# Performance work log

Measured on AMD Instinct MI355X. Metric: run time of the kernel, lower is better.

Reference implementation:

```python
import jax, jax.numpy as jnp
import numpy as np

N = 50000   # nodes per graph
E = 800000  # edges per graph (even, message() splits in half)
F = 100     # node/edge feature dim (init_count_size / init_emb_size)
D = 64      # hidden_dim3 = rule_graph_dim
W_SCALE = 0.05


def _mlp(x, w1, b1, w2, b2):
    return jax.nn.relu(x @ w1 + b1) @ w2 + b2


def _triple_conv(x, src, dst, ea, lw, lb, l2w, l2b, nn_fn):
    # PyG flow source_to_target: x_j = x[edge_index[0]], x_i = x[edge_index[1]]
    h = ea.shape[0] // 2
    x_j = x[src]
    x_i = x[dst]
    m1 = jax.nn.relu(jnp.concatenate([x_i[:h], ea[:h], x_j[:h]], 1) @ lw + lb)
    m2 = jax.nn.relu(jnp.concatenate([x_j[h:], ea[h:], x_i[h:]], 1) @ l2w + l2b)
    msgs = jnp.concatenate([m1, m2], 0)
    agg = jax.ops.segment_sum(msgs, dst, num_segments=x.shape[0])
    # eps = 0.0 buffer -> out = agg + (1+eps)*x = agg + x
    return nn_fn(agg + x)


def setup_inputs() -> dict:
    key = jax.random.key(0)
    ks = jax.random.split(key, 32)
    inp = {
        'features_1': jax.random.normal(ks[0], (N, F), jnp.float32),
        'edge_index_1': jax.random.randint(ks[1], (2, E), 0, N, jnp.int64 if jax.config.jax_enable_x64 else jnp.int32).astype(jnp.int32),
        'edge_attr_1': jax.random.normal(ks[2], (E, F), jnp.float32),
        'features_2': jax.random.normal(ks[3], (N, F), jnp.float32),
        'edge_index_2': jax.random.randint(ks[4], (2, E), 0, N, jnp.int32),
        'edge_attr_2': jax.random.normal(ks[5], (E, F), jnp.float32),
        'c1_lin_w': jax.random.normal(ks[6], (3 * F, F), jnp.float32) * W_SCALE,
        'c1_lin_b': jax.random.normal(ks[7], (F,), jnp.float32) * W_SCALE,
        'c1_lin2_w': jax.random.normal(ks[8], (3 * F, F), jnp.float32) * W_SCALE,
        'c1_lin2_b': jax.random.normal(ks[9], (F,), jnp.float32) * W_SCALE,
        'mlp1_w1': jax.random.normal(ks[10], (F, F), jnp.float32) * W_SCALE,
        'mlp1_b1': jax.random.normal(ks[11], (F,), jnp.float32) * W_SCALE,
        'mlp1_w2': jax.random.normal(ks[12], (F, F), jnp.float32) * W_SCALE,
        'mlp1_b2': jax.random.normal(ks[13], (F,), jnp.float32) * W_SCALE,
        'c2_lin_w': jax.random.normal(ks[14], (3 * F, F), jnp.float32) * W_SCALE,
        'c2_lin_b': jax.random.normal(ks[15], (F,), jnp.float32) * W_SCALE,
        'c2_lin2_w': jax.random.normal(ks[16], (3 * F, F), jnp.float32) * W_SCALE,
        'c2_lin2_b': jax.random.normal(ks[17], (F,), jnp.float32) * W_SCALE,
        'mlp2_w1': jax.random.normal(ks[18], (F, D), jnp.float32) * W_SCALE,
        'mlp2_b1': jax.random.normal(ks[19], (D,), jnp.float32) * W_SCALE,
        'mlp2_w2': jax.random.normal(ks[20], (D, D), jnp.float32) * W_SCALE,
        'mlp2_b2': jax.random.normal(ks[21], (D,), jnp.float32) * W_SCALE,
    }
    return inp


def reference(features_1, edge_index_1, edge_attr_1,
              features_2, edge_index_2, edge_attr_2,
              c1_lin_w, c1_lin_b, c1_lin2_w, c1_lin2_b,
              mlp1_w1, mlp1_b1, mlp1_w2, mlp1_b2,
              c2_lin_w, c2_lin_b, c2_lin2_w, c2_lin2_b,
              mlp2_w1, mlp2_b1, mlp2_w2, mlp2_b2):

    def conv_pass(x, ei, ea):
        src, dst = ei[0], ei[1]
        x = _triple_conv(x, src, dst, ea, c1_lin_w, c1_lin_b, c1_lin2_w, c1_lin2_b,
                         lambda z: _mlp(z, mlp1_w1, mlp1_b1, mlp1_w2, mlp1_b2))
        x = jax.nn.relu(x)
        x = _triple_conv(x, src, dst, ea, c2_lin_w, c2_lin_b, c2_lin2_w, c2_lin2_b,
                         lambda z: _mlp(z, mlp2_w1, mlp2_b1, mlp2_w2, mlp2_b2))
        return x

    f1 = conv_pass(features_1, edge_index_1, edge_attr_1)  # [N, D]
    f2 = conv_pass(features_2, edge_index_2, edge_attr_2)  # [N, D]
    # global_add_pool with a single batch id -> sum over nodes
    g1 = jnp.sum(f1, axis=0)
    g2 = jnp.sum(f2, axis=0)
    return jnp.stack([g1, g2], 0)  # [2, D]
```

## Files before the change

kernel.cpp:

```cpp
#include <hip/hip_runtime.h>

#define F 100
#define TS 256

typedef __attribute__((ext_vector_type(4))) unsigned short us4;
typedef __attribute__((ext_vector_type(8))) short short8;
typedef __attribute__((ext_vector_type(4))) float f32x4;

static __device__ __forceinline__ unsigned short f2bf(float f) {
    unsigned int u = __float_as_uint(f);
    unsigned int r = (u + 0x7FFF + ((u >> 16) & 1)) >> 16;
    return (unsigned short)r;
}
static __device__ __forceinline__ float bf2f(unsigned short u) {
    return __uint_as_float(((unsigned int)u) << 16);
}

__global__ __launch_bounds__(TS)
void hist2_kernel(const int* __restrict__ dst0, const int* __restrict__ dst1,
                  int h, int E, int N,
                  int* __restrict__ cnt1, int* __restrict__ cnt2)
{
    for (int idx = blockIdx.x * TS + threadIdx.x; idx < 2 * E; idx += gridDim.x * TS) {
        int g = idx >= E;
        int e = idx - g * E;
        int d = (g ? dst1 : dst0)[e];
        atomicAdd((e < h ? cnt1 : cnt2) + g * N + d, 1);
    }
}

__global__ __launch_bounds__(1024)
void scan4_kernel(const int* __restrict__ cnt1, const int* __restrict__ cnt2,
                  int* __restrict__ rp1, int* __restrict__ rp2, int n)
{
    const int which = blockIdx.x;
    const int hf = which >> 1, g = which & 1;
    const int* cnt = (hf ? cnt2 : cnt1) + g * n;
    int* rp = (hf ? rp2 : rp1) + g * (n + 1);
    __shared__ int buf[1024];
    __shared__ int carry_s;
    const int t = threadIdx.x;
    if (t == 0) carry_s = 0;
    __syncthreads();
    for (int base = 0; base < n; base += 8192) {
        int v[8], s = 0;
        #pragma unroll
        for (int j = 0; j < 8; ++j) {
            int idx = base + t * 8 + j;
            int x = (idx < n) ? cnt[idx] : 0;
            v[j] = s; s += x;
        }
        buf[t] = s;
        __syncthreads();
        for (int off = 1; off < 1024; off <<= 1) {
            int y = (t >= off) ? buf[t - off] : 0;
            __syncthreads();
            buf[t] += y;
            __syncthreads();
        }
        int excl = carry_s + buf[t] - s;
        #pragma unroll
        for (int j = 0; j < 8; ++j) {
            int idx = base + t * 8 + j;
            if (idx < n) rp[idx] = excl + v[j];
        }
        __syncthreads();
        if (t == 1023) carry_s += buf[1023];
        __syncthreads();
    }
    if (t == 0) rp[n] = carry_s;
}

__global__ __launch_bounds__(TS)
void scatter2_kernel(const int* __restrict__ src0, const int* __restrict__ dst0,
                     const int* __restrict__ src1, const int* __restrict__ dst1,
                     int h, int E, int N,
                     const int* __restrict__ rp1, const int* __restrict__ rp2,
                     int* __restrict__ cur1, int* __restrict__ cur2,
                     int* __restrict__ perm1, int* __restrict__ perm2,
                     int* __restrict__ es1, int* __restrict__ es2)
{
    for (int idx = blockIdx.x * TS + threadIdx.x; idx < 2 * E; idx += gridDim.x * TS) {
        int g = idx >= E;
        int e = idx - g * E;
        int d = (g ? dst1 : dst0)[e];
        int s = (g ? src1 : src0)[e];
        if (e < h) {
            int p = rp1[g * (N + 1) + d] + atomicAdd(&cur1[g * N + d], 1);
            perm1[g * h + p] = e; es1[g * h + p] = s + g * N;
        } else {
            int p = rp2[g * (N + 1) + d] + atomicAdd(&cur2[g * N + d], 1);
            perm2[g * h + p] = e; es2[g * h + p] = s + g * N;
        }
    }
}

__global__ __launch_bounds__(TS)
void pack_w_kernel(const float* w0, const float* w1, const float* w2, const float* w3,
                   unsigned short* __restrict__ Wp)
{
    int i = blockIdx.x * TS + threadIdx.x;
    if (i >= 12 * 112 * 128) return;
    int s = i / (112 * 128);
    int r = i - s * (112 * 128);
    int c = r >> 7, k = r & 127;
    int wi = s & 3, grp = s >> 2;
    const float* w = (wi == 0) ? w0 : (wi == 1) ? w1 : (wi == 2) ? w2 : w3;
    int off = (grp == 0) ? F : ((grp == 1) ? 0 : 2 * F);
    unsigned short v = 0;
    if (c < 100 && k < 100) v = f2bf(w[(off + k) * F + c]);
    Wp[i] = v;
}

__global__ __launch_bounds__(TS)
void pack_w2_kernel(const float* __restrict__ w, int K, int Nc, int ldb,
                    unsigned short* __restrict__ out)
{
    int i = blockIdx.x * TS + threadIdx.x;
    if (i >= 112 * 128) return;
    int c = i >> 7, k = i & 127;
    unsigned short v = 0;
    if (c < Nc && k < K) v = f2bf(w[k * ldb + c]);
    out[i] = v;
}

__global__ __launch_bounds__(TS)
void pack_x2_kernel(const float* __restrict__ x0, const float* __restrict__ x1,
                    int N, unsigned short* __restrict__ xb)
{
    const size_t total = (size_t)N * 2 * 32;
    for (size_t i = (size_t)blockIdx.x * TS + threadIdx.x; i < total; i += (size_t)gridDim.x * TS) {
        int n = (int)(i >> 5), q = (int)(i & 31);
        int g = n >= N;
        const float* x = g ? x1 : x0;
        int nl = n - g * N;
        us4 o = (us4){0, 0, 0, 0};
        if (q < 25) {
            float4 v = *(const float4*)&x[(size_t)nl * 100 + q * 4];
            o.x = f2bf(v.x); o.y = f2bf(v.y); o.z = f2bf(v.z); o.w = f2bf(v.w);
        }
        *(us4*)&xb[((size_t)n << 7) + q * 4] = o;
    }
}

__global__ __launch_bounds__(TS)
void gemm_node_mfma(const unsigned short* __restrict__ xb,
                    const unsigned short* __restrict__ B0, const unsigned short* __restrict__ B1,
                    const unsigned short* __restrict__ B2, const unsigned short* __restrict__ B3,
                    unsigned short* __restrict__ NTb,
                    int M)
{
    const int t = threadIdx.x, lane = t & 63, wv = t >> 6;
    const int rA = lane & 15, kg = lane >> 4;
    const unsigned short* Bp[4] = {B0, B1, B2, B3};
    const int ntiles = (M + 15) >> 4;
    for (int tile = blockIdx.x * 4 + wv; tile < ntiles; tile += gridDim.x * 4) {
        const int base = tile << 4;
        const int arow = min(base + rA, M - 1);
        short8 A[4];
        #pragma unroll
        for (int ks = 0; ks < 4; ++ks)
            A[ks] = *(const short8*)&xb[((size_t)arow << 7) + ks * 32 + kg * 8];
        const int row = base + rA;
        #pragma unroll
        for (int sel = 0; sel < 4; ++sel) {
            const unsigned short* B = Bp[sel];
            f32x4 C[7];
            #pragma unroll
            for (int nf = 0; nf < 7; ++nf) C[nf] = (f32x4){0.f, 0.f, 0.f, 0.f};
            #pragma unroll
            for (int ks = 0; ks < 4; ++ks) {
                #pragma unroll
                for (int nf = 0; nf < 7; ++nf) {
                    short8 Bf = *(const short8*)&B[(size_t)(rA + nf * 16) * 128 + ks * 32 + kg * 8];
                    C[nf] = __builtin_amdgcn_mfma_f32_16x16x32_bf16(Bf, A[ks], C[nf], 0, 0, 0);
                }
            }
            if (row < M) {
                #pragma unroll
                for (int nf = 0; nf < 7; ++nf) {
                    const int cb = nf * 16 + kg * 4;
                    if (cb < 100) {
                        us4 o;
                        o.x = f2bf(C[nf][0]); o.y = f2bf(C[nf][1]);
                        o.z = f2bf(C[nf][2]); o.w = f2bf(C[nf][3]);
                        *(us4*)&NTb[(size_t)row * 400 + sel * 100 + cb] = o;
                    }
                }
            }
        }
    }
}

__global__ __launch_bounds__(TS)
void gemm_edge_quad(const float* __restrict__ ea0, const float* __restrict__ ea1,
                    const int* __restrict__ perm1, const int* __restrict__ perm2,
                    const unsigned short* __restrict__ Wp,
                    unsigned short* __restrict__ P1A, unsigned short* __restrict__ P2A,
                    unsigned short* __restrict__ P1B, unsigned short* __restrict__ P2B,
                    int h, int HG)
{
    __shared__ unsigned short sA[2][64][136];
    const int t = threadIdx.x, lane = t & 63, wv = t >> 6;
    const int rA = lane & 15, kg = lane >> 4;
    const int M = 2 * h;
    const int ngrp = M >> 6;
    const int r_loc = t >> 2, sub = t & 3;

    const int half = blockIdx.x >= HG;
    const int bid = blockIdx.x - (half ? HG : 0);
    const int* perm = half ? perm2 : perm1;
    const unsigned short* W0 = Wp + (size_t)(half ? 1 : 0) * (112 * 128);
    const unsigned short* W1 = Wp + (size_t)(half ? 3 : 2) * (112 * 128);
    unsigned short* P0 = half ? P1B : P1A;
    unsigned short* P1 = half ? P2B : P2A;

    int grp = bid;
    if (grp >= ngrp) return;

    {
        const int grow = (grp << 6) + r_loc;
        const int g = grow >= h;
        const int e = perm[grow];
        const float* ea = (g ? ea1 : ea0) + (size_t)e * 100;
        float4 raw[7];
        #pragma unroll
        for (int j = 0; j < 7; ++j) {
            const int q = sub + 4 * j;
            if (q < 25) raw[j] = *(const float4*)&ea[q * 4];
        }
        #pragma unroll
        for (int j = 0; j < 8; ++j) {
            const int q = sub + 4 * j;
            us4 o = (us4){0, 0, 0, 0};
            if (j < 7 && q < 25) {
                o.x = f2bf(raw[j].x); o.y = f2bf(raw[j].y);
                o.z = f2bf(raw[j].z); o.w = f2bf(raw[j].w);
            }
            if (q < 32) *(us4*)&sA[0][r_loc][q * 4] = o;
        }
    }
    __syncthreads();

    int cur = 0;
    while (true) {
        const int nxt = grp + HG;
        const bool more = nxt < ngrp;

        float4 raw[7];
        if (more) {
            const int grow = (nxt << 6) + r_loc;
            const int g = grow >= h;
            const int e = perm[grow];
            const float* ea = (g ? ea1 : ea0) + (size_t)e * 100;
            #pragma unroll
            for (int j = 0; j < 7; ++j) {
                const int q = sub + 4 * j;
                if (q < 25) raw[j] = *(const float4*)&ea[q * 4];
            }
        }

        {
            const int lrow = wv * 16 + rA;
            short8 A[4];
            #pragma unroll
            for (int ks = 0; ks < 4; ++ks)
                A[ks] = *(const short8*)&sA[cur][lrow][ks * 32 + kg * 8];

            f32x4 C0[7], C1[7];
            #pragma unroll
            for (int nf = 0; nf < 7; ++nf) {
                C0[nf] = (f32x4){0.f, 0.f, 0.f, 0.f};
                C1[nf] = (f32x4){0.f, 0.f, 0.f, 0.f};
            }
            #pragma unroll
            for (int ks = 0; ks < 4; ++ks) {
                #pragma unroll
                for (int nf = 0; nf < 7; ++nf) {
                    short8 B0f = *(const short8*)&W0[(size_t)(rA + nf * 16) * 128 + ks * 32 + kg * 8];
                    C0[nf] = __builtin_amdgcn_mfma_f32_16x16x32_bf16(B0f, A[ks], C0[nf], 0, 0, 0);
                    short8 B1f = *(const short8*)&W1[(size_t)(rA + nf * 16) * 128 + ks * 32 + kg * 8];
                    C1[nf] = __builtin_amdgcn_mfma_f32_16x16x32_bf16(B1f, A[ks], C1[nf], 0, 0, 0);
                }
            }
            const int row = (grp << 6) + lrow;
            #pragma unroll
            for (int nf = 0; nf < 7; ++nf) {
                const int cb = nf * 16 + kg * 4;
                if (cb < 100) {
                    us4 o0, o1;
                    o0.x = f2bf(C0[nf][0]); o0.y = f2bf(C0[nf][1]);
                    o0.z = f2bf(C0[nf][2]); o0.w = f2bf(C0[nf][3]);
                    o1.x = f2bf(C1[nf][0]); o1.y = f2bf(C1[nf][1]);
                    o1.z = f2bf(C1[nf][2]); o1.w = f2bf(C1[nf][3]);
                    *(us4*)&P0[(size_t)row * 100 + cb] = o0;
                    *(us4*)&P1[(size_t)row * 100 + cb] = o1;
                }
            }
        }

        if (!more) break;

        #pragma unroll
        for (int j = 0; j < 8; ++j) {
            const int q = sub + 4 * j;
            us4 o = (us4){0, 0, 0, 0};
            if (j < 7 && q < 25) {
                o.x = f2bf(raw[j].x); o.y = f2bf(raw[j].y);
                o.z = f2bf(raw[j].z); o.w = f2bf(raw[j].w);
            }
            if (q < 32) *(us4*)&sA[cur ^ 1][r_loc][q * 4] = o;
        }
        __syncthreads();
        cur ^= 1; grp = nxt;
    }
}

__global__ __launch_bounds__(TS)
void seg_reduce_fused(const unsigned short* __restrict__ PA,
                      const unsigned short* __restrict__ PB,
                      const int* __restrict__ es1, const int* __restrict__ es2,
                      const int* __restrict__ rp1, const int* __restrict__ rp2,
                      const float* __restrict__ cb, const float* __restrict__ cb2,
                      const unsigned short* __restrict__ NTb,
                      const float* __restrict__ x0, const float* __restrict__ x1,
                      const unsigned short* __restrict__ xbin,
                      unsigned short* __restrict__ Ab,
                      int N, int h, int mode)
{
    const int gid = blockIdx.x * TS + threadIdx.x;
    const int n = gid >> 6;
    if (n >= 2 * N) return;
    const int q6 = gid & 63;
    const int sub = q6 >> 5, q = q6 & 31;
    const int c4 = q * 4;
    if (q >= 25) {
        if (sub == 0) *(us4*)&Ab[((size_t)n << 7) + c4] = (us4){0, 0, 0, 0};
        return;
    }
    const int g = n >= N;
    const int nl = n - g * N;

    float d1x, d1y, d1z, d1w, d2x, d2y, d2z, d2w;
    {
        const us4 vd1 = *(const us4*)&NTb[(size_t)n * 400 + 0 * 100 + c4];
        const float4 b1 = *(const float4*)&cb[c4];
        d1x = bf2f(vd1.x) + b1.x; d1y = bf2f(vd1.y) + b1.y;
        d1z = bf2f(vd1.z) + b1.z; d1w = bf2f(vd1.w) + b1.w;
        const us4 vd2 = *(const us4*)&NTb[(size_t)n * 400 + 3 * 100 + c4];
        const float4 b2 = *(const float4*)&cb2[c4];
        d2x = bf2f(vd2.x) + b2.x; d2y = bf2f(vd2.y) + b2.y;
        d2z = bf2f(vd2.z) + b2.z; d2w = bf2f(vd2.w) + b2.w;
    }
    const int* rpg1 = rp1 + g * (N + 1);
    const int* rpg2 = rp2 + g * (N + 1);
    int pos1 = max(rpg1[nl], 0) + g * h + sub;
    const int end1 = min(rpg1[nl + 1], h) + g * h;
    int pos2 = max(rpg2[nl], 0) + g * h + sub;
    const int end2 = min(rpg2[nl + 1], h) + g * h;

    float ax = 0.f, ay = 0.f, az = 0.f, aw = 0.f;

    const int len1 = (end1 - pos1 + 1) >> 1;
    const int len2 = (end2 - pos2 + 1) >> 1;

    const int common = min(len1, len2);
    #pragma unroll 2
    for (int i = 0; i < common; ++i) {
        const int i1 = pos1 + 2 * i;
        const int i2 = pos2 + 2 * i;
        const int s1 = es1[i1];
        const int s2 = es2[i2];
        const us4 pv1 = *(const us4*)&PA[(size_t)i1 * 100 + c4];
        const us4 pv2 = *(const us4*)&PB[(size_t)i2 * 100 + c4];
        const us4 v1 = *(const us4*)&NTb[(size_t)s1 * 400 + 1 * 100 + c4];
        const us4 v2 = *(const us4*)&NTb[(size_t)s2 * 400 + 2 * 100 + c4];
        ax += fmaxf(bf2f(pv1.x) + bf2f(v1.x) + d1x, 0.f)
            + fmaxf(bf2f(pv2.x) + bf2f(v2.x) + d2x, 0.f);
        ay += fmaxf(bf2f(pv1.y) + bf2f(v1.y) + d1y, 0.f)
            + fmaxf(bf2f(pv2.y) + bf2f(v2.y) + d2y, 0.f);
        az += fmaxf(bf2f(pv1.z) + bf2f(v1.z) + d1z, 0.f)
            + fmaxf(bf2f(pv2.z) + bf2f(v2.z) + d2z, 0.f);
        aw += fmaxf(bf2f(pv1.w) + bf2f(v1.w) + d1w, 0.f)
            + fmaxf(bf2f(pv2.w) + bf2f(v2.w) + d2w, 0.f);
    }
    pos1 += 2 * common; pos2 += 2 * common;

    #pragma unroll 2
    for (; pos1 < end1; pos1 += 2) {
        const int s = es1[pos1];
        const us4 pv = *(const us4*)&PA[(size_t)pos1 * 100 + c4];
        const us4 vs = *(const us4*)&NTb[(size_t)s * 400 + 1 * 100 + c4];
        ax += fmaxf(bf2f(pv.x) + bf2f(vs.x) + d1x, 0.f);
        ay += fmaxf(bf2f(pv.y) + bf2f(vs.y) + d1y, 0.f);
        az += fmaxf(bf2f(pv.z) + bf2f(vs.z) + d1z, 0.f);
        aw += fmaxf(bf2f(pv.w) + bf2f(vs.w) + d1w, 0.f);
    }
    #pragma unroll 2
    for (; pos2 < end2; pos2 += 2) {
        const int s = es2[pos2];
        const us4 pv = *(const us4*)&PB[(size_t)pos2 * 100 + c4];
        const us4 vs = *(const us4*)&NTb[(size_t)s * 400 + 2 * 100 + c4];
        ax += fmaxf(bf2f(pv.x) + bf2f(vs.x) + d2x, 0.f);
        ay += fmaxf(bf2f(pv.y) + bf2f(vs.y) + d2y, 0.f);
        az += fmaxf(bf2f(pv.z) + bf2f(vs.z) + d2z, 0.f);
        aw += fmaxf(bf2f(pv.w) + bf2f(vs.w) + d2w, 0.f);
    }

    ax += __shfl_xor(ax, 32);
    ay += __shfl_xor(ay, 32);
    az += __shfl_xor(az, 32);
    aw += __shfl_xor(aw, 32);
    if (sub != 0) return;

    float4 xv;
    if (mode == 0) {
        const float* x = g ? x1 : x0;
        xv = *(const float4*)&x[(size_t)nl * 100 + c4];
    } else {
        const us4 v = *(const us4*)&xbin[((size_t)n << 7) + c4];
        xv.x = bf2f(v.x); xv.y = bf2f(v.y); xv.z = bf2f(v.z); xv.w = bf2f(v.w);
    }
    us4 o;
    o.x = f2bf(ax + xv.x); o.y = f2bf(ay + xv.y);
    o.z = f2bf(az + xv.z); o.w = f2bf(aw + xv.w);
    *(us4*)&Ab[((size_t)n << 7) + c4] = o;
}

__global__ __launch_bounds__(TS)
void gemm_mlp_bf16out(const unsigned short* __restrict__ Ab,
                      const unsigned short* __restrict__ Wp,
                      const float* __restrict__ bias,
                      unsigned short* __restrict__ out,
                      int M, int Nc)
{
    const int t = threadIdx.x, lane = t & 63, wv = t >> 6;
    const int rA = lane & 15, kg = lane >> 4;
    const int ntiles = (M + 15) >> 4;
    for (int tile = blockIdx.x * 4 + wv; tile < ntiles; tile += gridDim.x * 4) {
        const int base = tile << 4;
        const int arow = min(base + rA, M - 1);
        f32x4 C[7];
        #pragma unroll
        for (int nf = 0; nf < 7; ++nf) C[nf] = (f32x4){0.f, 0.f, 0.f, 0.f};
        #pragma unroll
        for (int ks = 0; ks < 4; ++ks) {
            short8 A = *(const short8*)&Ab[((size_t)arow << 7) + ks * 32 + kg * 8];
            #pragma unroll
            for (int nf = 0; nf < 7; ++nf) {
                short8 B = *(const short8*)&Wp[(size_t)(rA + nf * 16) * 128 + ks * 32 + kg * 8];
                C[nf] = __builtin_amdgcn_mfma_f32_16x16x32_bf16(B, A, C[nf], 0, 0, 0);
            }
        }
        const int row = base + rA;
        if (row < M) {
            #pragma unroll
            for (int nf = 0; nf < 7; ++nf) {
                const int cb = nf * 16 + kg * 4;
                us4 o = (us4){0, 0, 0, 0};
                if (cb < Nc) {
                    float4 bv = *(const float4*)&bias[cb];
                    o.x = f2bf(fmaxf(C[nf][0] + bv.x, 0.f));
                    o.y = f2bf(fmaxf(C[nf][1] + bv.y, 0.f));
                    o.z = f2bf(fmaxf(C[nf][2] + bv.z, 0.f));
                    o.w = f2bf(fmaxf(C[nf][3] + bv.w, 0.f));
                }
                *(us4*)&out[((size_t)row << 7) + cb] = o;
            }
            *(us4*)&out[((size_t)row << 7) + 112 + kg * 4] = (us4){0, 0, 0, 0};
        }
    }
}

__global__ __launch_bounds__(TS)
void gemm_mlp_f32out(const unsigned short* __restrict__ Ab,
                     const unsigned short* __restrict__ Wp,
                     const float* __restrict__ bias,
                     float* __restrict__ out,
                     int M)
{
    const int t = threadIdx.x, lane = t & 63, wv = t >> 6;
    const int rA = lane & 15, kg = lane >> 4;
    const int ntiles = (M + 15) >> 4;
    for (int tile = blockIdx.x * 4 + wv; tile < ntiles; tile += gridDim.x * 4) {
        const int base = tile << 4;
        const int arow = min(base + rA, M - 1);
        f32x4 C[4];
        #pragma unroll
        for (int nf = 0; nf < 4; ++nf) C[nf] = (f32x4){0.f, 0.f, 0.f, 0.f};
        #pragma unroll
        for (int ks = 0; ks < 2; ++ks) {
            short8 A = *(const short8*)&Ab[((size_t)arow << 7) + ks * 32 + kg * 8];
            #pragma unroll
            for (int nf = 0; nf < 4; ++nf) {
                short8 B = *(const short8*)&Wp[(size_t)(rA + nf * 16) * 128 + ks * 32 + kg * 8];
                C[nf] = __builtin_amdgcn_mfma_f32_16x16x32_bf16(B, A, C[nf], 0, 0, 0);
            }
        }
        const int row = base + rA;
        if (row < M) {
            #pragma unroll
            for (int nf = 0; nf < 4; ++nf) {
                const int cb = nf * 16 + kg * 4;
                float4 bv = *(const float4*)&bias[cb];
                float4 o;
                o.x = C[nf][0] + bv.x; o.y = C[nf][1] + bv.y;
                o.z = C[nf][2] + bv.z; o.w = C[nf][3] + bv.w;
                *(float4*)&out[(size_t)row * 64 + cb] = o;
            }
        }
    }
}

__global__ __launch_bounds__(TS)
void colsum2_kernel(const float* __restrict__ Fm, int N, float* __restrict__ out)
{
    __shared__ float red[4][2][64];
    const int t = threadIdx.x;
    const int c = t & 63, rg = t >> 6;
    float s0 = 0.f, s1 = 0.f;
    const int M = 2 * N;
    for (int r = blockIdx.x * 4 + rg; r < M; r += gridDim.x * 4) {
        float v = Fm[(size_t)r * 64 + c];
        if (r < N) s0 += v; else s1 += v;
    }
    red[rg][0][c] = s0; red[rg][1][c] = s1;
    __syncthreads();
    if (rg == 0) {
        atomicAdd(&out[c],      red[0][0][c] + red[1][0][c] + red[2][0][c] + red[3][0][c]);
        atomicAdd(&out[64 + c], red[0][1][c] + red[1][1][c] + red[2][1][c] + red[3][1][c]);
    }
}

extern "C" void kernel_launch(void* const* d_in, const int* in_sizes, int n_in,
                              void* d_out, int out_size, void* d_ws, size_t ws_size,
                              hipStream_t stream)
{
    const int N = in_sizes[0] / F;
    const int E = in_sizes[1] / 2;
    const int h = E / 2;
    const int N2 = 2 * N, h2 = 2 * h;

    unsigned short* NTb  = (unsigned short*)d_ws;
    unsigned short* P1A = NTb + (size_t)N2 * 400;
    unsigned short* P1B = P1A + (size_t)h2 * 100;
    unsigned short* P2A = P1B + (size_t)h2 * 100;
    unsigned short* P2B = P2A + (size_t)h2 * 100;
    unsigned short* xb  = P2B + (size_t)h2 * 100;
    unsigned short* X1b = xb + (size_t)N2 * 128;
    unsigned short* Ab  = X1b + (size_t)N2 * 128;
    unsigned short* Hb  = Ab + (size_t)N2 * 128;
    float* F2  = (float*)(Hb + (size_t)N2 * 128);
    int* rp1   = (int*)(F2 + (size_t)N2 * 64);
    int* rp2   = rp1 + 2 * (N + 1);
    int* cnt1  = rp2 + 2 * (N + 1);
    int* cnt2  = cnt1 + N2;
    int* perm1 = cnt2 + N2;
    int* perm2 = perm1 + h2;
    int* es1   = perm2 + h2;
    int* es2   = es1 + h2;
    unsigned short* Wp = (unsigned short*)(es2 + h2);
    unsigned short* Wm = Wp + (size_t)12 * 112 * 128;

    const float* x0g0 = (const float*)d_in[0];
    const int*   ei0  = (const int*)d_in[1];
    const float* ea0  = (const float*)d_in[2];
    const float* x0g1 = (const float*)d_in[3];
    const int*   ei1  = (const int*)d_in[4];
    const float* ea1  = (const float*)d_in[5];
    const float* c1w  = (const float*)d_in[6];
    const float* c1b  = (const float*)d_in[7];
    const float* c1w2 = (const float*)d_in[8];
    const float* c1b2 = (const float*)d_in[9];
    const float* m1w1 = (const float*)d_in[10];
    const float* m1b1 = (const float*)d_in[11];
    const float* m1w2 = (const float*)d_in[12];
    const float* m1b2 = (const float*)d_in[13];
    const float* c2w  = (const float*)d_in[14];
    const float* c2b  = (const float*)d_in[15];
    const float* c2w2 = (const float*)d_in[16];
    const float* c2b2 = (const float*)d_in[17];
    const float* m2w1 = (const float*)d_in[18];
    const float* m2b1 = (const float*)d_in[19];
    const float* m2w2 = (const float*)d_in[20];
    const float* m2b2 = (const float*)d_in[21];

    hipMemsetAsync(d_out, 0, (size_t)out_size * sizeof(float), stream);

    const dim3 blk(TS);
    const size_t SL = (size_t)112 * 128;
    pack_w_kernel<<<(12 * 112 * 128 + TS - 1) / TS, blk, 0, stream>>>(c1w, c1w2, c2w, c2w2, Wp);
    pack_w2_kernel<<<56, blk, 0, stream>>>(m1w1, 100, 100, 100, Wm + 0 * SL);
    pack_w2_kernel<<<56, blk, 0, stream>>>(m1w2, 100, 100, 100, Wm + 1 * SL);
    pack_w2_kernel<<<56, blk, 0, stream>>>(m2w1, 100,  64,  64, Wm + 2 * SL);
    pack_w2_kernel<<<56, blk, 0, stream>>>(m2w2,  64,  64,  64, Wm + 3 * SL);

    hipMemsetAsync(cnt1, 0, 2 * (size_t)N2 * sizeof(int), stream);
    hist2_kernel<<<2048, blk, 0, stream>>>(ei0 + E, ei1 + E, h, E, N, cnt1, cnt2);
    scan4_kernel<<<4, 1024, 0, stream>>>(cnt1, cnt2, rp1, rp2, N);
    hipMemsetAsync(cnt1, 0, 2 * (size_t)N2 * sizeof(int), stream);
    scatter2_kernel<<<2048, blk, 0, stream>>>(ei0, ei0 + E, ei1, ei1 + E, h, E, N,
                                              rp1, rp2, cnt1, cnt2, perm1, perm2, es1, es2);
    pack_x2_kernel<<<2048, blk, 0, stream>>>(x0g0, x0g1, N, xb);

    gemm_edge_quad<<<4096, blk, 0, stream>>>(ea0, ea1, perm1, perm2, Wp,
                                             P1A, P2A, P1B, P2B, h, 2048);

    const int nblkR = (N2 * 64 + TS - 1) / TS;
    for (int conv = 0; conv < 2; ++conv) {
        const float* cb  = conv ? c2b  : c1b;
        const float* cb2 = conv ? c2b2 : c1b2;
        const unsigned short* xin = conv ? X1b : xb;
        const int iw  = conv ? 2 : 0;
        const int iw2 = conv ? 3 : 1;
        const unsigned short* PA = conv ? P2A : P1A;
        const unsigned short* PB = conv ? P2B : P1B;

        gemm_node_mfma<<<2048, blk, 0, stream>>>(xin,
            Wp + (size_t)(4 + iw)  * SL, Wp + (size_t)(8 + iw)  * SL,
            Wp + (size_t)(4 + iw2) * SL, Wp + (size_t)(8 + iw2) * SL,
            NTb, N2);

        seg_reduce_fused<<<nblkR, blk, 0, stream>>>(PA, PB, es1, es2, rp1, rp2,
                                                    cb, cb2, NTb,
                                                    x0g0, x0g1, X1b, Ab,
                                                    N, h, conv);

        if (conv == 0) {
            gemm_mlp_bf16out<<<2048, blk, 0, stream>>>(Ab, Wm + 0 * SL, m1b1, Hb,  N2, 100);
            gemm_mlp_bf16out<<<2048, blk, 0, stream>>>(Hb, Wm + 1 * SL, m1b2, X1b, N2, 100);
        } else {
            gemm_mlp_bf16out<<<2048, blk, 0, stream>>>(Ab, Wm + 2 * SL, m2b1, Hb, N2, 64);
            gemm_mlp_f32out<<<2048, blk, 0, stream>>>(Hb, Wm + 3 * SL, m2b2, F2, N2);
        }
    }
    colsum2_kernel<<<512, blk, 0, stream>>>(F2, N, (float*)d_out);
    (void)ws_size; (void)n_in;
}
```

Measured before the change: 1.360 ms.

## Fuse two-layer node MLPs through LDS and fold final column sum into GEMM

Merges the two per-layer MLP GEMM launches into one kernel, with each wave staging its 16-row hidden tile in shared memory instead of writing and re-reading a global hidden buffer. For the second conv, the final layer's output is reduced on the fly into per-graph column sums with shuffles plus shared and global atomics, which drops the F2 buffer and the separate colsum kernel. The grid now covers one tile per wave rather than a fixed 2048 blocks. Tail handling assumes N2 is a multiple of 16, and the per-tile graph split assumes N is a multiple of 16.

```diff
diff --git a/kernel.cpp b/kernel.cpp
--- a/kernel.cpp
+++ b/kernel.cpp
@@ -428,108 +428,166 @@
 }
 
 __global__ __launch_bounds__(TS)
-void gemm_mlp_bf16out(const unsigned short* __restrict__ Ab,
-                      const unsigned short* __restrict__ Wp,
-                      const float* __restrict__ bias,
-                      unsigned short* __restrict__ out,
-                      int M, int Nc)
-{
+void gemm_mlp2_bf16(const unsigned short* __restrict__ Ab,
+                    const unsigned short* __restrict__ W1, const float* __restrict__ b1,
+                    const unsigned short* __restrict__ W2, const float* __restrict__ b2,
+                    unsigned short* __restrict__ out, int M)
+{
+    __shared__ unsigned short sH[4][16][136];
     const int t = threadIdx.x, lane = t & 63, wv = t >> 6;
     const int rA = lane & 15, kg = lane >> 4;
-    const int ntiles = (M + 15) >> 4;
+    const int ntiles = M >> 4;
+    for (int tile = blockIdx.x * 4 + wv; tile < ntiles; tile += gridDim.x * 4) {
+        const int row = (tile << 4) + rA;
+        f32x4 C[7];
+        #pragma unroll
+        for (int nf = 0; nf < 7; ++nf) C[nf] = (f32x4){0.f, 0.f, 0.f, 0.f};
+        #pragma unroll
+        for (int ks = 0; ks < 4; ++ks) {
+            short8 A = *(const short8*)&Ab[((size_t)row << 7) + ks * 32 + kg * 8];
+            #pragma unroll
+            for (int nf = 0; nf < 7; ++nf) {
+                short8 B = *(const short8*)&W1[(size_t)(rA + nf * 16) * 128 + ks * 32 + kg * 8];
+                C[nf] = __builtin_amdgcn_mfma_f32_16x16x32_bf16(B, A, C[nf], 0, 0, 0);
+            }
+        }
+        #pragma unroll
+        for (int nf = 0; nf < 7; ++nf) {
+            const int cbp = nf * 16 + kg * 4;
+            us4 o = (us4){0, 0, 0, 0};
+            if (cbp < 100) {
+                float4 bv = *(const float4*)&b1[cbp];
+                o.x = f2bf(fmaxf(C[nf][0] + bv.x, 0.f));
+                o.y = f2bf(fmaxf(C[nf][1] + bv.y, 0.f));
+                o.z = f2bf(fmaxf(C[nf][2] + bv.z, 0.f));
+                o.w = f2bf(fmaxf(C[nf][3] + bv.w, 0.f));
+            }
+            *(us4*)&sH[wv][rA][cbp] = o;
+        }
+        *(us4*)&sH[wv][rA][112 + kg * 4] = (us4){0, 0, 0, 0};
+        f32x4 D[7];
+        #pragma unroll
+        for (int nf = 0; nf < 7; ++nf) D[nf] = (f32x4){0.f, 0.f, 0.f, 0.f};
+        #pragma unroll
+        for (int ks = 0; ks < 4; ++ks) {
+            short8 A2 = *(const short8*)&sH[wv][rA][ks * 32 + kg * 8];
+            #pragma unroll
+            for (int nf = 0; nf < 7; ++nf) {
+                short8 B = *(const short8*)&W2[(size_t)(rA + nf * 16) * 128 + ks * 32 + kg * 8];
+                D[nf] = __builtin_amdgcn_mfma_f32_16x16x32_bf16(B, A2, D[nf], 0, 0, 0);
+            }
+        }
+        #pragma unroll
+        for (int nf = 0; nf < 7; ++nf) {
+            const int cbp = nf * 16 + kg * 4;
+            us4 o = (us4){0, 0, 0, 0};
+            if (cbp < 100) {
+                float4 bv = *(const float4*)&b2[cbp];
+                o.x = f2bf(fmaxf(D[nf][0] + bv.x, 0.f));
+                o.y = f2bf(fmaxf(D[nf][1] + bv.y, 0.f));
+                o.z = f2bf(fmaxf(D[nf][2] + bv.z, 0.f));
+                o.w = f2bf(fmaxf(D[nf][3] + bv.w, 0.f));
+            }
+            *(us4*)&out[((size_t)row << 7) + cbp] = o;
+        }
+        *(us4*)&out[((size_t)row << 7) + 112 + kg * 4] = (us4){0, 0, 0, 0};
+    }
+}
+
+__global__ __launch_bounds__(TS)
+void gemm_mlp2_colsum(const unsigned short* __restrict__ Ab,
+                      const unsigned short* __restrict__ W1, const float* __restrict__ b1,
+                      const unsigned short* __restrict__ W2, const float* __restrict__ b2,
+                      float* __restrict__ outp, int M, int N)
+{
+    __shared__ unsigned short sH[4][16][136];
+    __shared__ float sums[128];
+    const int t = threadIdx.x, lane = t & 63, wv = t >> 6;
+    const int rA = lane & 15, kg = lane >> 4;
+    if (t < 128) sums[t] = 0.f;
+    __syncthreads();
+
+    f32x4 acc0[4], acc1[4];
+    #pragma unroll
+    for (int nf = 0; nf < 4; ++nf) {
+        acc0[nf] = (f32x4){0.f, 0.f, 0.f, 0.f};
+        acc1[nf] = (f32x4){0.f, 0.f, 0.f, 0.f};
+    }
+
+    const int ntiles = M >> 4;
     for (int tile = blockIdx.x * 4 + wv; tile < ntiles; tile += gridDim.x * 4) {
         const int base = tile << 4;
-        const int arow = min(base + rA, M - 1);
-        f32x4 C[7];
-        #pragma unroll
-        for (int nf = 0; nf < 7; ++nf) C[nf] = (f32x4){0.f, 0.f, 0.f, 0.f};
+        const int row = base + rA;
+        f32x4 C[4];
+        #pragma unroll
+        for (int nf = 0; nf < 4; ++nf) C[nf] = (f32x4){0.f, 0.f, 0.f, 0.f};
         #pragma unroll
         for (int ks = 0; ks < 4; ++ks) {
-            short8 A = *(const short8*)&Ab[((size_t)arow << 7) + ks * 32 + kg * 8];
-            #pragma unroll
-            for (int nf = 0; nf < 7; ++nf) {
-                short8 B = *(const short8*)&Wp[(size_t)(rA + nf * 16) * 128 + ks * 32 + kg * 8];
+            short8 A = *(const short8*)&Ab[((size_t)row << 7) + ks * 32 + kg * 8];
+            #pragma unroll
+            for (int nf = 0; nf < 4; ++nf) {
+                short8 B = *(const short8*)&W1[(size_t)(rA + nf * 16) * 128 + ks * 32 + kg * 8];
                 C[nf] = __builtin_amdgcn_mfma_f32_16x16x32_bf16(B, A, C[nf], 0, 0, 0);
             }
         }
-        const int row = base + rA;
-        if (row < M) {
-            #pragma unroll
-            for (int nf = 0; nf < 7; ++nf) {
-                const int cb = nf * 16 + kg * 4;
-                us4 o = (us4){0, 0, 0, 0};
-                if (cb < Nc) {
-                    float4 bv = *(const float4*)&bias[cb];
-                    o.x = f2bf(fmaxf(C[nf][0] + bv.x, 0.f));
-                    o.y = f2bf(fmaxf(C[nf][1] + bv.y, 0.f));
-                    o.z = f2bf(fmaxf(C[nf][2] + bv.z, 0.f));
-                    o.w = f2bf(fmaxf(C[nf][3] + bv.w, 0.f));
-                }
-                *(us4*)&out[((size_t)row << 7) + cb] = o;
-            }
-            *(us4*)&out[((size_t)row << 7) + 112 + kg * 4] = (us4){0, 0, 0, 0};
-        }
-    }
-}
-
-__global__ __launch_bounds__(TS)
-void gemm_mlp_f32out(const unsigned short* __restrict__ Ab,
-                     const unsigned short* __restrict__ Wp,
-                     const float* __restrict__ bias,
-                     float* __restrict__ out,
-                     int M)
-{
-    const int t = threadIdx.x, lane = t & 63, wv = t >> 6;
-    const int rA = lane & 15, kg = lane >> 4;
-    const int ntiles = (M + 15) >> 4;
-    for (int tile = blockIdx.x * 4 + wv; tile < ntiles; tile += gridDim.x * 4) {
-        const int base = tile << 4;
-        const int arow = min(base + rA, M - 1);
-        f32x4 C[4];
-        #pragma unroll
-        for (int nf = 0; nf < 4; ++nf) C[nf] = (f32x4){0.f, 0.f, 0.f, 0.f};
+        #pragma unroll
+        for (int nf = 0; nf < 4; ++nf) {
+            const int cbp = nf * 16 + kg * 4;
+            float4 bv = *(const float4*)&b1[cbp];
+            us4 o;
+            o.x = f2bf(fmaxf(C[nf][0] + bv.x, 0.f));
+            o.y = f2bf(fmaxf(C[nf][1] + bv.y, 0.f));
+            o.z = f2bf(fmaxf(C[nf][2] + bv.z, 0.f));
+            o.w = f2bf(fmaxf(C[nf][3] + bv.w, 0.f));
+            *(us4*)&sH[wv][rA][cbp] = o;
+        }
+        f32x4 D[4];
+        #pragma unroll
+        for (int nf = 0; nf < 4; ++nf) D[nf] = (f32x4){0.f, 0.f, 0.f, 0.f};
         #pragma unroll
         for (int ks = 0; ks < 2; ++ks) {
-            short8 A = *(const short8*)&Ab[((size_t)arow << 7) + ks * 32 + kg * 8];
+            short8 A2 = *(const short8*)&sH[wv][rA][ks * 32 + kg * 8];
             #pragma unroll
             for (int nf = 0; nf < 4; ++nf) {
-                short8 B = *(const short8*)&Wp[(size_t)(rA + nf * 16) * 128 + ks * 32 + kg * 8];
-                C[nf] = __builtin_amdgcn_mfma_f32_16x16x32_bf16(B, A, C[nf], 0, 0, 0);
-            }
-        }
-        const int row = base + rA;
-        if (row < M) {
+                short8 B = *(const short8*)&W2[(size_t)(rA + nf * 16) * 128 + ks * 32 + kg * 8];
+                D[nf] = __builtin_amdgcn_mfma_f32_16x16x32_bf16(B, A2, D[nf], 0, 0, 0);
+            }
+        }
+        if (base >= N) {
             #pragma unroll
             for (int nf = 0; nf < 4; ++nf) {
-                const int cb = nf * 16 + kg * 4;
-                float4 bv = *(const float4*)&bias[cb];
-                float4 o;
-                o.x = C[nf][0] + bv.x; o.y = C[nf][1] + bv.y;
-                o.z = C[nf][2] + bv.z; o.w = C[nf][3] + bv.w;
-                *(float4*)&out[(size_t)row * 64 + cb] = o;
-            }
-        }
-    }
-}
-
-__global__ __launch_bounds__(TS)
-void colsum2_kernel(const float* __restrict__ Fm, int N, float* __restrict__ out)
-{
-    __shared__ float red[4][2][64];
-    const int t = threadIdx.x;
-    const int c = t & 63, rg = t >> 6;
-    float s0 = 0.f, s1 = 0.f;
-    const int M = 2 * N;
-    for (int r = blockIdx.x * 4 + rg; r < M; r += gridDim.x * 4) {
-        float v = Fm[(size_t)r * 64 + c];
-        if (r < N) s0 += v; else s1 += v;
-    }
-    red[rg][0][c] = s0; red[rg][1][c] = s1;
+                float4 bv = *(const float4*)&b2[nf * 16 + kg * 4];
+                acc1[nf][0] += D[nf][0] + bv.x; acc1[nf][1] += D[nf][1] + bv.y;
+                acc1[nf][2] += D[nf][2] + bv.z; acc1[nf][3] += D[nf][3] + bv.w;
+            }
+        } else {
+            #pragma unroll
+            for (int nf = 0; nf < 4; ++nf) {
+                float4 bv = *(const float4*)&b2[nf * 16 + kg * 4];
+                acc0[nf][0] += D[nf][0] + bv.x; acc0[nf][1] += D[nf][1] + bv.y;
+                acc0[nf][2] += D[nf][2] + bv.z; acc0[nf][3] += D[nf][3] + bv.w;
+            }
+        }
+    }
+
+    #pragma unroll
+    for (int nf = 0; nf < 4; ++nf) {
+        #pragma unroll
+        for (int r = 0; r < 4; ++r) {
+            float v0 = acc0[nf][r], v1 = acc1[nf][r];
+            v0 += __shfl_xor(v0, 1); v0 += __shfl_xor(v0, 2);
+            v0 += __shfl_xor(v0, 4); v0 += __shfl_xor(v0, 8);
+            v1 += __shfl_xor(v1, 1); v1 += __shfl_xor(v1, 2);
+            v1 += __shfl_xor(v1, 4); v1 += __shfl_xor(v1, 8);
+            if (rA == 0) {
+                const int f = nf * 16 + kg * 4 + r;
+                atomicAdd(&sums[f], v0);
+                atomicAdd(&sums[64 + f], v1);
+            }
+        }
+    }
     __syncthreads();
-    if (rg == 0) {
-        atomicAdd(&out[c],      red[0][0][c] + red[1][0][c] + red[2][0][c] + red[3][0][c]);
-        atomicAdd(&out[64 + c], red[0][1][c] + red[1][1][c] + red[2][1][c] + red[3][1][c]);
-    }
+    if (t < 128) atomicAdd(&outp[t], sums[t]);
 }
 
 extern "C" void kernel_launch(void* const* d_in, const int* in_sizes, int n_in,
@@ -607,6 +665,7 @@
                                              P1A, P2A, P1B, P2B, h, 2048);
 
     const int nblkR = (N2 * 64 + TS - 1) / TS;
+    const int nblkM = (N2 / 16 + 3) / 4;
     for (int conv = 0; conv < 2; ++conv) {
         const float* cb  = conv ? c2b  : c1b;
         const float* cb2 = conv ? c2b2 : c1b2;
@@ -627,13 +686,13 @@
                                                     N, h, conv);
 
         if (conv == 0) {
-            gemm_mlp_bf16out<<<2048, blk, 0, stream>>>(Ab, Wm + 0 * SL, m1b1, Hb,  N2, 100);
-            gemm_mlp_bf16out<<<2048, blk, 0, stream>>>(Hb, Wm + 1 * SL, m1b2, X1b, N2, 100);
+            gemm_mlp2_bf16<<<nblkM, blk, 0, stream>>>(Ab, Wm + 0 * SL, m1b1,
+                                                      Wm + 1 * SL, m1b2, X1b, N2);
         } else {
-            gemm_mlp_bf16out<<<2048, blk, 0, stream>>>(Ab, Wm + 2 * SL, m2b1, Hb, N2, 64);
-            gemm_mlp_f32out<<<2048, blk, 0, stream>>>(Hb, Wm + 3 * SL, m2b2, F2, N2);
-        }
-    }
-    colsum2_kernel<<<512, blk, 0, stream>>>(F2, N, (float*)d_out);
+            gemm_mlp2_colsum<<<nblkM, blk, 0, stream>>>(Ab, Wm + 2 * SL, m2b1,
+                                                        Wm + 3 * SL, m2b2,
+                                                        (float*)d_out, N2, N);
+        }
+    }
     (void)ws_size; (void)n_in;
 }
```

Measured after the change: 1.334 ms. About the same (-2.0%).
